# Kernel tuning notes

Measured on AMD Instinct MI355X. Metric: run time of the kernel, lower is better.

The kernel has to match this reference:

```python
import jax, jax.numpy as jnp
import numpy as np

N_LAYERS = 2
H = 16                      # num_heads
ARW = (1.0, 1.0)            # att_residual_weight
MCB = (0.0, 1.0)            # mask_clip_balancer
LN_EPS = 1e-5


def _ln(x, g, b):
    mu = jnp.mean(x, axis=-1, keepdims=True)
    var = jnp.mean(jnp.square(x - mu), axis=-1, keepdims=True)
    return (x - mu) * jax.lax.rsqrt(var + LN_EPS) * g + b


def _quick_gelu(u):
    return u * jax.nn.sigmoid(1.702 * u)


def setup_inputs() -> dict:
    key = jax.random.key(0)
    ks = jax.random.split(key, 8)
    L, B, C = 577, 8, 1024
    d_ff = 4 * C
    inp = {
        'x': jax.random.normal(ks[0], (L, B, C), jnp.float32),
        'att_bias': jax.random.normal(ks[1], (N_LAYERS, B * H, L, L), jnp.float32),
        'ln1_g': jnp.ones((N_LAYERS, C), jnp.float32),
        'ln1_b': jnp.zeros((N_LAYERS, C), jnp.float32),
        'in_w': 0.02 * jax.random.normal(ks[2], (N_LAYERS, 3 * C, C), jnp.float32),
        'in_b': jnp.zeros((N_LAYERS, 3 * C), jnp.float32),
        'out_w': 0.02 * jax.random.normal(ks[3], (N_LAYERS, C, C), jnp.float32),
        'out_b': jnp.zeros((N_LAYERS, C), jnp.float32),
        'ln2_g': jnp.ones((N_LAYERS, C), jnp.float32),
        'ln2_b': jnp.zeros((N_LAYERS, C), jnp.float32),
        'fc1_w': 0.02 * jax.random.normal(ks[4], (N_LAYERS, d_ff, C), jnp.float32),
        'fc1_b': jnp.zeros((N_LAYERS, d_ff), jnp.float32),
        'fc2_w': 0.02 * jax.random.normal(ks[5], (N_LAYERS, C, d_ff), jnp.float32),
        'fc2_b': jnp.zeros((N_LAYERS, C), jnp.float32),
    }
    return inp


def reference(x, att_bias, ln1_g, ln1_b, in_w, in_b, out_w, out_b,
              ln2_g, ln2_b, fc1_w, fc1_b, fc2_w, fc2_b):
    L, B, C = x.shape
    d = C // H
    scale = d ** -0.5  # custom_att_factor is None
    for i in range(N_LAYERS):
        # --- custom CSA attention ---
        h = _ln(x, ln1_g[i], ln1_b[i])                              # [L,B,C]
        qkv = jnp.einsum('lbc,fc->lbf', h, in_w[i]) + in_b[i]       # [L,B,3C]
        q, k, v = jnp.split(qkv, 3, axis=-1)
        to_heads = lambda t: t.reshape(L, B, H, d).transpose(1, 2, 0, 3)  # [B,H,L,d]
        q, k, v = to_heads(q), to_heads(k), to_heads(v)
        bias = att_bias[i].reshape(B, H, L, L)
        q_attn = bias + scale * jnp.einsum('bhld,bhmd->bhlm', q, q)
        k_attn = bias + scale * jnp.einsum('bhld,bhmd->bhlm', k, k)
        attn = jax.nn.softmax(q_attn, axis=-1) + jax.nn.softmax(k_attn, axis=-1)
        attn = attn * 0.5                                           # norm_att=True
        attn = jnp.mean(attn, axis=1, keepdims=True)                # avg_att=True -> [B,1,L,L]
        out = jnp.matmul(attn, v)                                   # broadcast over H -> [B,H,L,d]
        out = MCB[0] * v + MCB[1] * out
        out = out.transpose(2, 0, 1, 3).reshape(L, B, C)
        out = jnp.einsum('lbc,oc->lbo', out, out_w[i]) + out_b[i]
        x = ARW[0] * x + ARW[1] * out
        # --- MLP residual ---
        h2 = _ln(x, ln2_g[i], ln2_b[i])
        u = _quick_gelu(jnp.einsum('lbc,fc->lbf', h2, fc1_w[i]) + fc1_b[i])
        x = x + jnp.einsum('lbf,cf->lbc', u, fc2_w[i]) + fc2_b[i]
    return x
```

## Files before the change

### kernel.cpp

```cpp
#include <hip/hip_runtime.h>

typedef float f32x4 __attribute__((ext_vector_type(4)));
typedef __bf16 bf16x8 __attribute__((ext_vector_type(8)));

#define L_SEQ 577
#define BB 8
#define CC 1024
#define HH 16
#define ROWS (L_SEQ*BB)

static __device__ __forceinline__ ushort f2b(float f) {
  unsigned u = __float_as_uint(f);
  u += 0x7fffu + ((u >> 16) & 1u);
  return (ushort)(u >> 16);
}

static __device__ __forceinline__ void gld16(const void* g, void* l) {
  __builtin_amdgcn_global_load_lds((const __attribute__((address_space(1))) void*)g,
                                   (__attribute__((address_space(3))) void*)l, 16, 0, 0);
}

__global__ void cvt4_kernel(const float* __restrict__ s0, ushort* __restrict__ d0, int n0,
                            const float* __restrict__ s1, ushort* __restrict__ d1, int n1,
                            const float* __restrict__ s2, ushort* __restrict__ d2, int n2,
                            const float* __restrict__ s3, ushort* __restrict__ d3, int n3)
{
  int i = blockIdx.x * blockDim.x + threadIdx.x;
  const float* src; ushort* dst;
  if (i < n0)                { src = s0; dst = d0; }
  else if ((i -= n0) < n1)   { src = s1; dst = d1; }
  else if ((i -= n1) < n2)   { src = s2; dst = d2; }
  else if ((i -= n2) < n3)   { src = s3; dst = d3; }
  else return;
  float4 v = *(const float4*)(src + (size_t)i * 4);
  ushort4 o;
  o.x = f2b(v.x); o.y = f2b(v.y); o.z = f2b(v.z); o.w = f2b(v.w);
  *(ushort4*)(dst + (size_t)i * 4) = o;
}

template<int NP, bool DOLN>
__global__ __launch_bounds__(256)
void ln_resid_kernel(const float* __restrict__ xsrc, const float* __restrict__ parts,
                     const float* __restrict__ cbias,
                     const float* __restrict__ g, const float* __restrict__ be,
                     float* __restrict__ xdst, ushort* __restrict__ hout)
{
  const int row = blockIdx.x;
  const int t = threadIdx.x;
  float4 v = *(const float4*)(xsrc + (size_t)row * CC + t * 4);
  if (NP > 0) {
    float4 c4 = *(const float4*)(cbias + t * 4);
    v.x += c4.x; v.y += c4.y; v.z += c4.z; v.w += c4.w;
    #pragma unroll
    for (int p = 0; p < NP; ++p) {
      float4 pv = *(const float4*)(parts + ((size_t)p * ROWS + row) * CC + t * 4);
      v.x += pv.x; v.y += pv.y; v.z += pv.z; v.w += pv.w;
    }
  }
  *(float4*)(xdst + (size_t)row * CC + t * 4) = v;
  if (DOLN) {
    float s  = v.x + v.y + v.z + v.w;
    float s2 = v.x*v.x + v.y*v.y + v.z*v.z + v.w*v.w;
    #pragma unroll
    for (int sd = 1; sd < 64; sd <<= 1) { s += __shfl_xor(s, sd, 64); s2 += __shfl_xor(s2, sd, 64); }
    __shared__ float ps[4], ps2[4];
    const int w = t >> 6;
    if ((t & 63) == 0) { ps[w] = s; ps2[w] = s2; }
    __syncthreads();
    s  = ps[0] + ps[1] + ps[2] + ps[3];
    s2 = ps2[0] + ps2[1] + ps2[2] + ps2[3];
    const float mean = s * (1.f / 1024.f);
    const float var  = s2 * (1.f / 1024.f) - mean * mean;
    const float rstd = rsqrtf(var + 1e-5f);
    float4 gv = *(const float4*)(g + t * 4);
    float4 bv = *(const float4*)(be + t * 4);
    ushort4 o;
    o.x = f2b((v.x - mean) * rstd * gv.x + bv.x);
    o.y = f2b((v.y - mean) * rstd * gv.y + bv.y);
    o.z = f2b((v.z - mean) * rstd * gv.z + bv.z);
    o.w = f2b((v.w - mean) * rstd * gv.w + bv.w);
    *(ushort4*)(hout + (size_t)row * CC + t * 4) = o;
  }
}

__global__ __launch_bounds__(256)
void vt_kernel(const ushort* __restrict__ qkv, ushort* __restrict__ vt)
{
  __shared__ ushort tile[32][33];
  const int lt = blockIdx.x * 32;
  const int nt = blockIdx.y * 32;
  const int b  = blockIdx.z;
  const int tx = threadIdx.x & 31;
  const int ty = threadIdx.x >> 5;
  #pragma unroll
  for (int p = 0; p < 4; ++p) {
    int l = lt + ty + p * 8;
    ushort v = 0;
    if (l < L_SEQ) v = qkv[((size_t)l * BB + b) * 3072 + 2048 + nt + tx];
    tile[ty + p * 8][tx] = v;
  }
  __syncthreads();
  #pragma unroll
  for (int p = 0; p < 4; ++p) {
    int n = nt + ty + p * 8;
    int l = lt + tx;
    vt[((size_t)b * 1024 + n) * 608 + l] = tile[tx][ty + p * 8];
  }
}

__global__ __launch_bounds__(512, 2)
void attn_kernel(const ushort* __restrict__ qkv,
                 const float* __restrict__ bias,
                 ushort* __restrict__ attnp)
{
  __shared__ float2 red[2][2][8][16];
  __shared__ ushort sm[16][612];
  const int t = threadIdx.x;
  const int lane = t & 63;
  const int w = t >> 6;
  const int fr = lane & 15;
  const int lq = lane >> 4;
  const int id = blockIdx.x;
  const int b  = id & 7;
  const int rem = id >> 3;
  const int rb = rem % 37;
  const int hg = rem / 37;
  const int r0 = rb * 16;
  const int rowl = min(r0 + fr, L_SEQ - 1);
  const size_t rbase = ((size_t)rowl * BB + b) * 3072;
  const int kc = lq * 8;

  size_t cbs_[5];
  int c0_[5];
  #pragma unroll
  for (int it = 0; it < 5; ++it) {
    const int nt = w + it * 8;
    const int crow = min(nt * 16 + fr, L_SEQ - 1);
    cbs_[it] = ((size_t)crow * BB + b) * 3072;
    c0_[it] = nt * 16 + lq * 4;
  }

  float acc[5][4];
  #pragma unroll
  for (int it = 0; it < 5; ++it)
    #pragma unroll
    for (int r = 0; r < 4; ++r) acc[it][r] = 0.f;

  for (int h4 = 0; h4 < 4; ++h4) {
    const int h = hg * 4 + h4;
    const int qoff = h * 64;
    const int koff = CC + h * 64;
    const bf16x8 rfq0 = *(const bf16x8*)(qkv + rbase + qoff + kc);
    const bf16x8 rfq1 = *(const bf16x8*)(qkv + rbase + qoff + 32 + kc);
    const bf16x8 rfk0 = *(const bf16x8*)(qkv + rbase + koff + kc);
    const bf16x8 rfk1 = *(const bf16x8*)(qkv + rbase + koff + 32 + kc);
    const float* brow = bias + (((size_t)(b * HH + h)) * L_SEQ + rowl) * L_SEQ;

    float bs[5][4];
    #pragma unroll
    for (int it = 0; it < 5; ++it)
      #pragma unroll
      for (int r = 0; r < 4; ++r) bs[it][r] = brow[min(c0_[it] + r, L_SEQ - 1)];
    bf16x8 cq0[5], cq1[5], ck0[5], ck1[5];
    #pragma unroll
    for (int it = 0; it < 5; ++it) {
      const ushort* cp = qkv + cbs_[it];
      cq0[it] = *(const bf16x8*)(cp + qoff + kc);
      cq1[it] = *(const bf16x8*)(cp + qoff + 32 + kc);
      ck0[it] = *(const bf16x8*)(cp + koff + kc);
      ck1[it] = *(const bf16x8*)(cp + koff + 32 + kc);
    }

    float sq[5][4], sk[5][4];
    #pragma unroll
    for (int it = 0; it < 5; ++it) {
      f32x4 dq = {0.f, 0.f, 0.f, 0.f};
      f32x4 dk = {0.f, 0.f, 0.f, 0.f};
      dq = __builtin_amdgcn_mfma_f32_16x16x32_bf16(cq0[it], rfq0, dq, 0, 0, 0);
      dq = __builtin_amdgcn_mfma_f32_16x16x32_bf16(cq1[it], rfq1, dq, 0, 0, 0);
      dk = __builtin_amdgcn_mfma_f32_16x16x32_bf16(ck0[it], rfk0, dk, 0, 0, 0);
      dk = __builtin_amdgcn_mfma_f32_16x16x32_bf16(ck1[it], rfk1, dk, 0, 0, 0);
      #pragma unroll
      for (int r = 0; r < 4; ++r) {
        const bool cv = (c0_[it] + r < L_SEQ);
        sq[it][r] = cv ? (bs[it][r] + 0.125f * dq[r]) : -1e30f;
        sk[it][r] = cv ? (bs[it][r] + 0.125f * dk[r]) : -1e30f;
      }
    }
    float mwq = -1e30f, mwk = -1e30f;
    #pragma unroll
    for (int it = 0; it < 5; ++it)
      #pragma unroll
      for (int r = 0; r < 4; ++r) { mwq = fmaxf(mwq, sq[it][r]); mwk = fmaxf(mwk, sk[it][r]); }
    mwq = fmaxf(mwq, __shfl_xor(mwq, 16, 64)); mwq = fmaxf(mwq, __shfl_xor(mwq, 32, 64));
    mwk = fmaxf(mwk, __shfl_xor(mwk, 16, 64)); mwk = fmaxf(mwk, __shfl_xor(mwk, 32, 64));
    float swq = 0.f, swk = 0.f;
    #pragma unroll
    for (int it = 0; it < 5; ++it)
      #pragma unroll
      for (int r = 0; r < 4; ++r) {
        sq[it][r] = __expf(sq[it][r] - mwq); swq += sq[it][r];
        sk[it][r] = __expf(sk[it][r] - mwk); swk += sk[it][r];
      }
    swq += __shfl_xor(swq, 16, 64); swq += __shfl_xor(swq, 32, 64);
    swk += __shfl_xor(swk, 16, 64); swk += __shfl_xor(swk, 32, 64);
    const int p = h4 & 1;
    if (lane < 16) {
      red[p][0][w][lane] = make_float2(mwq, swq);
      red[p][1][w][lane] = make_float2(mwk, swk);
    }
    __syncthreads();
    float mq = -1e30f, mk = -1e30f;
    #pragma unroll
    for (int ww = 0; ww < 8; ++ww) {
      mq = fmaxf(mq, red[p][0][ww][fr].x);
      mk = fmaxf(mk, red[p][1][ww][fr].x);
    }
    float smq = 0.f, smk = 0.f;
    #pragma unroll
    for (int ww = 0; ww < 8; ++ww) {
      const float2 pq = red[p][0][ww][fr];
      const float2 pk = red[p][1][ww][fr];
      smq += pq.y * __expf(pq.x - mq);
      smk += pk.y * __expf(pk.x - mk);
    }
    const float fq = 0.03125f * __expf(mwq - mq) / smq;
    const float fk = 0.03125f * __expf(mwk - mk) / smk;
    #pragma unroll
    for (int it = 0; it < 5; ++it)
      #pragma unroll
      for (int r = 0; r < 4; ++r) acc[it][r] += sq[it][r] * fq + sk[it][r] * fk;
  }

  #pragma unroll
  for (int it = 0; it < 5; ++it) {
    if (c0_[it] < 608) {
      ushort4 o;
      o.x = f2b(acc[it][0]); o.y = f2b(acc[it][1]);
      o.z = f2b(acc[it][2]); o.w = f2b(acc[it][3]);
      *(ushort4*)&sm[fr][c0_[it]] = o;
    }
  }
  __syncthreads();
  ushort* dst = attnp + ((size_t)hg * 8 + b) * 608 * 608 + (size_t)r0 * 608;
  for (int j = t; j < 16 * 152; j += 512) {
    const int row = j / 152;
    const int c4 = (j % 152) * 4;
    if (r0 + row < L_SEQ)
      *(ushort4*)(dst + (size_t)row * 608 + c4) = *(const ushort4*)&sm[row][c4];
  }
}

__global__ __launch_bounds__(256)
void attn_combine(const ushort* __restrict__ attnp, ushort* __restrict__ attn)
{
  const int t = threadIdx.x;
  if (t >= 152) return;
  const int l = blockIdx.x;
  const int b = blockIdx.y;
  const int c0 = t * 4;
  const size_t base = ((size_t)b * 608 + l) * 608 + c0;
  const size_t hs = (size_t)8 * 608 * 608;
  float s[4] = {0.f, 0.f, 0.f, 0.f};
  #pragma unroll
  for (int p = 0; p < 4; ++p) {
    ushort4 v = *(const ushort4*)(attnp + p * hs + base);
    s[0] += __uint_as_float((unsigned)v.x << 16);
    s[1] += __uint_as_float((unsigned)v.y << 16);
    s[2] += __uint_as_float((unsigned)v.z << 16);
    s[3] += __uint_as_float((unsigned)v.w << 16);
  }
  ushort4 o;
  const bool lv = (l < L_SEQ);
  o.x = (lv && c0 + 0 < L_SEQ) ? f2b(s[0]) : (ushort)0;
  o.y = (lv && c0 + 1 < L_SEQ) ? f2b(s[1]) : (ushort)0;
  o.z = (lv && c0 + 2 < L_SEQ) ? f2b(s[2]) : (ushort)0;
  o.w = (lv && c0 + 3 < L_SEQ) ? f2b(s[3]) : (ushort)0;
  *(ushort4*)(attn + base) = o;
}

__global__ __launch_bounds__(256, 2)
void av_gemm(const ushort* __restrict__ A, int lda, int Arows, long aStride,
             const ushort* __restrict__ B, int ldb, long bStride,
             int M, int K,
             ushort* __restrict__ outb, int ldo)
{
  __shared__ __align__(16) ushort As[128 * 32];
  __shared__ __align__(16) ushort Bs[128 * 32];
  const int t = threadIdx.x;
  const int lane = t & 63;
  const int w = t >> 6;
  const int bm = blockIdx.x, bn = blockIdx.y, bz = blockIdx.z;
  const ushort* Ab = A + (long)bz * aStride;
  const ushort* Bb = B + (long)bz * bStride;
  const int srow = t >> 2;
  const int sc = (t & 3) * 8;
  const int wr = (w >> 1) * 64;
  const int wc = (w & 1) * 64;
  const int am1 = Arows - 1;
  f32x4 acc[4][4] = {};

  const int r0a = bm * 128 + srow;
  const int r0b = bn * 128 + srow;
  for (int kt = 0; kt < K; kt += 32) {
    __syncthreads();
    gld16(Ab + (size_t)min(r0a, am1) * lda + kt + sc, (void*)(As + t * 8));
    gld16(Ab + (size_t)min(r0a + 64, am1) * lda + kt + sc, (void*)(As + 2048 + t * 8));
    gld16(Bb + (size_t)r0b * ldb + kt + sc, (void*)(Bs + t * 8));
    gld16(Bb + (size_t)(r0b + 64) * ldb + kt + sc, (void*)(Bs + 2048 + t * 8));
    asm volatile("s_waitcnt vmcnt(0)" ::: "memory");
    __syncthreads();
    bf16x8 av[4], bv[4];
    const int fr = lane & 15;
    const int kc = (lane >> 4) * 8;
    #pragma unroll
    for (int m = 0; m < 4; ++m) av[m] = *(const bf16x8*)(As + (wr + m * 16 + fr) * 32 + kc);
    #pragma unroll
    for (int n = 0; n < 4; ++n) bv[n] = *(const bf16x8*)(Bs + (wc + n * 16 + fr) * 32 + kc);
    #pragma unroll
    for (int m = 0; m < 4; ++m)
      #pragma unroll
      for (int n = 0; n < 4; ++n)
        acc[m][n] = __builtin_amdgcn_mfma_f32_16x16x32_bf16(av[m], bv[n], acc[m][n], 0, 0, 0);
  }
  const int rbase = wr + (lane >> 4) * 4;
  const int cbase = wc + (lane & 15);
  #pragma unroll
  for (int n = 0; n < 4; ++n) {
    const int gn = bn * 128 + cbase + n * 16;
    #pragma unroll
    for (int m = 0; m < 4; ++m) {
      f32x4 d = acc[m][n];
      #pragma unroll
      for (int r = 0; r < 4; ++r) {
        const int gm = bm * 128 + rbase + m * 16 + r;
        if (gm < M) outb[((size_t)gm * 8 + bz) * ldo + gn] = f2b(d[r]);
      }
    }
  }
}

#define RD_A8(BOFS, MH) \
  _Pragma("unroll") for (int ks = 0; ks < 2; ++ks) \
  _Pragma("unroll") for (int m = 0; m < 4; ++m) \
    Af[ks][m] = rdA(BOFS, MH, ks, m);

#define RD_B4(BOFS, NH) \
  _Pragma("unroll") for (int ks = 0; ks < 2; ++ks) \
  _Pragma("unroll") for (int n = 0; n < 2; ++n) \
    Bf[NH][ks][n] = rdB(BOFS, NH, ks, n);

#define MFQ(MH, NH) \
  _Pragma("unroll") for (int ks = 0; ks < 2; ++ks) \
  _Pragma("unroll") for (int m = 0; m < 4; ++m) \
  _Pragma("unroll") for (int n = 0; n < 2; ++n) \
    acc[(MH)*4+m][(NH)*2+n] = __builtin_amdgcn_mfma_f32_16x16x32_bf16( \
        Af[ks][m], Bf[NH][ks][n], acc[(MH)*4+m][(NH)*2+n], 0, 0, 0);

#define BARO() \
  __builtin_amdgcn_sched_barrier(0); \
  __builtin_amdgcn_s_barrier(); \
  asm volatile("s_waitcnt lgkmcnt(0)" ::: "memory"); \
  __builtin_amdgcn_sched_barrier(0); \
  __builtin_amdgcn_s_setprio(1);

#define MF_END() \
  __builtin_amdgcn_s_setprio(0); \
  __builtin_amdgcn_sched_barrier(0); \
  __builtin_amdgcn_s_barrier();

template<int EPI>
__global__ __launch_bounds__(512, 2)
void gemm8(const ushort* __restrict__ Ap, int lda, int Arows,
           const ushort* __restrict__ Bp, int ldb,
           int M, int Ksplit,
           const float* __restrict__ bias,
           ushort* __restrict__ outb, float* __restrict__ outf, int ldo)
{
  __shared__ __align__(16) char smem[131072];
  const int t = threadIdx.x;
  const int lane = t & 63;
  const int w = t >> 6;
  const int wm = w >> 2, wn = w & 3;
  const int gx = gridDim.x;
  const int nwg = gx * gridDim.y;
  int id = blockIdx.y * gx + blockIdx.x;
  {
    const int q8 = nwg >> 3, r8 = nwg & 7;
    const int xcd = id & 7, pos = id >> 3;
    id = (xcd < r8 ? xcd * (q8 + 1) : r8 * (q8 + 1) + (xcd - r8) * q8) + pos;
  }
  const int bm = id % gx, bn = id / gx;
  const int bz = blockIdx.z;
  const int k0 = bz * Ksplit;
  const int iters = Ksplit >> 7;
  const int fr = lane & 15, lq = lane >> 4;

  f32x4 acc[8][4] = {};
  bf16x8 Af[2][4];
  bf16x8 Bf[2][2][2];

  const int rowj0 = t >> 3,        cbj0 = t & 7;
  const int rowj1 = (t + 512) >> 3, cbj1 = (t + 512) & 7;
  const ushort* pA[2][2]; const ushort* pB[2][2];
  #pragma unroll
  for (int h = 0; h < 2; ++h) {
    pA[h][0] = Ap + (size_t)min(bm*256 + h*128 + rowj0, Arows-1) * lda + k0 + ((cbj0 ^ (rowj0 & 7)) << 3);
    pA[h][1] = Ap + (size_t)min(bm*256 + h*128 + rowj1, Arows-1) * lda + k0 + ((cbj1 ^ (rowj1 & 7)) << 3);
    pB[h][0] = Bp + (size_t)(bn*256 + h*128 + rowj0) * ldb + k0 + ((cbj0 ^ (rowj0 & 7)) << 3);
    pB[h][1] = Bp + (size_t)(bn*256 + h*128 + rowj1) * ldb + k0 + ((cbj1 ^ (rowj1 & 7)) << 3);
  }

  auto stA = [&](int kt, int bofs, int h) {
    gld16(pA[h][0] + kt * 64, smem + bofs + h * 16384 + t * 16);
    gld16(pA[h][1] + kt * 64, smem + bofs + h * 16384 + (t + 512) * 16);
  };
  auto stB = [&](int kt, int bofs, int h) {
    gld16(pB[h][0] + kt * 64, smem + bofs + 32768 + h * 16384 + t * 16);
    gld16(pB[h][1] + kt * 64, smem + bofs + 32768 + h * 16384 + (t + 512) * 16);
  };
  auto rdA = [&](int bofs, int mh, int ks, int m) -> bf16x8 {
    const int rl = wm * 64 + m * 16 + fr;
    const int cb = (ks * 4 + lq) ^ (fr & 7);
    return *(const bf16x8*)(smem + bofs + mh * 16384 + rl * 128 + cb * 16);
  };
  auto rdB = [&](int bofs, int nh, int ks, int n) -> bf16x8 {
    const int rl = wn * 32 + n * 16 + fr;
    const int cb = (ks * 4 + lq) ^ (fr & 7);
    return *(const bf16x8*)(smem + bofs + 32768 + nh * 16384 + rl * 128 + cb * 16);
  };

  stA(0, 0, 0); stB(0, 0, 0); stB(0, 0, 1); stA(0, 0, 1);
  stA(1, 65536, 0); stB(1, 65536, 1); stA(1, 65536, 1);
  asm volatile("s_waitcnt vmcnt(6)" ::: "memory");
  __builtin_amdgcn_sched_barrier(0);
  __builtin_amdgcn_s_barrier();

  for (int i = 0; i < iters; ++i) {
    const bool more = (i + 1 < iters);
    const int kt2 = 2 * i + 2;
    RD_A8(0, 0) RD_B4(0, 0)
    stB(2 * i + 1, 65536, 0);
    BARO(); MFQ(0, 0) MF_END();
    RD_B4(0, 1)
    if (more) stA(kt2, 0, 0);
    BARO(); MFQ(0, 1) MF_END();
    RD_A8(0, 1)
    if (more) stB(kt2, 0, 1);
    BARO(); MFQ(1, 1) MF_END();
    if (more) stA(kt2, 0, 1);
    BARO(); MFQ(1, 0)
    __builtin_amdgcn_s_setprio(0);
    if (more) { asm volatile("s_waitcnt vmcnt(6)" ::: "memory"); }
    else      { asm volatile("s_waitcnt vmcnt(0)" ::: "memory"); }
    __builtin_amdgcn_sched_barrier(0);
    __builtin_amdgcn_s_barrier();
    RD_A8(65536, 0) RD_B4(65536, 0)
    if (more) stB(kt2, 0, 0);
    BARO(); MFQ(0, 0) MF_END();
    RD_B4(65536, 1)
    if (more) stA(2 * i + 3, 65536, 0);
    BARO(); MFQ(0, 1) MF_END();
    RD_A8(65536, 1)
    if (more) stB(2 * i + 3, 65536, 1);
    BARO(); MFQ(1, 1) MF_END();
    if (more) stA(2 * i + 3, 65536, 1);
    BARO(); MFQ(1, 0)
    __builtin_amdgcn_s_setprio(0);
    if (more) { asm volatile("s_waitcnt vmcnt(6)" ::: "memory"); }
    __builtin_amdgcn_sched_barrier(0);
    __builtin_amdgcn_s_barrier();
  }

  #pragma unroll
  for (int mh = 0; mh < 2; ++mh)
  #pragma unroll
  for (int nh = 0; nh < 2; ++nh)
  #pragma unroll
  for (int n = 0; n < 2; ++n) {
    const int gn = bn * 256 + nh * 128 + wn * 32 + n * 16 + fr;
    const float bval = (EPI == 4) ? 0.f : bias[gn];
    #pragma unroll
    for (int m = 0; m < 4; ++m) {
      f32x4 d = acc[mh * 4 + m][nh * 2 + n];
      #pragma unroll
      for (int r = 0; r < 4; ++r) {
        const int gm = bm * 256 + mh * 128 + wm * 64 + m * 16 + lq * 4 + r;
        if (gm < M) {
          if (EPI == 0) {
            outb[(size_t)gm * ldo + gn] = f2b(d[r] + bval);
          } else if (EPI == 1) {
            float v0 = d[r] + bval;
            outb[(size_t)gm * ldo + gn] = f2b(v0 / (1.f + __expf(-1.702f * v0)));
          } else {
            outf[((size_t)bz * M + gm) * ldo + gn] = d[r];
          }
        }
      }
    }
  }
}

extern "C" void kernel_launch(void* const* d_in, const int* in_sizes, int n_in,
                              void* d_out, int out_size, void* d_ws, size_t ws_size,
                              hipStream_t stream)
{
  (void)in_sizes; (void)n_in; (void)out_size; (void)ws_size;
  const float* x_in  = (const float*)d_in[0];
  const float* attb  = (const float*)d_in[1];
  const float* ln1_g = (const float*)d_in[2];
  const float* ln1_b = (const float*)d_in[3];
  const float* in_w  = (const float*)d_in[4];
  const float* in_b  = (const float*)d_in[5];
  const float* out_w = (const float*)d_in[6];
  const float* out_b = (const float*)d_in[7];
  const float* ln2_g = (const float*)d_in[8];
  const float* ln2_b = (const float*)d_in[9];
  const float* fc1_w = (const float*)d_in[10];
  const float* fc1_b = (const float*)d_in[11];
  const float* fc2_w = (const float*)d_in[12];
  const float* fc2_b = (const float*)d_in[13];
  float* x = (float*)d_out;

  char* ws = (char*)d_ws;
  size_t off = 0;
  auto alloc = [&](size_t bytes) -> void* {
    void* p = ws + off; off += (bytes + 255) & ~(size_t)255; return p;
  };
  ushort* wIn   = (ushort*)alloc(2ull * 3072 * 1024 * 2);
  ushort* wOut  = (ushort*)alloc(2ull * 1024 * 1024 * 2);
  ushort* wF1   = (ushort*)alloc(2ull * 4096 * 1024 * 2);
  ushort* wF2   = (ushort*)alloc(2ull * 4096 * 1024 * 2);
  ushort* hbuf  = (ushort*)alloc((size_t)ROWS * 1024 * 2);
  ushort* qkv   = (ushort*)alloc((size_t)ROWS * 3072 * 2);
  ushort* vt    = (ushort*)alloc((size_t)8 * 1024 * 608 * 2);
  ushort* attn  = (ushort*)alloc((size_t)8 * 608 * 608 * 2);
  ushort* attnp = (ushort*)alloc((size_t)4 * 8 * 608 * 608 * 2);
  ushort* outlb = (ushort*)alloc((size_t)ROWS * 1024 * 2);
  float*  pbuf  = (float*)alloc((size_t)4 * ROWS * 1024 * 4);
  ushort* ubuf  = qkv;

  cvt4_kernel<<<(1572864 + 524288 + 2097152 + 2097152 + 255) / 256, 256, 0, stream>>>(
      in_w,  wIn,  1572864,
      out_w, wOut, 524288,
      fc1_w, wF1,  2097152,
      fc2_w, wF2,  2097152);
  ln_resid_kernel<0, true><<<ROWS, 256, 0, stream>>>(x_in, nullptr, nullptr,
      ln1_g, ln1_b, x, hbuf);

  for (int i = 0; i < 2; ++i) {
    gemm8<0><<<dim3(19, 12, 1), 512, 0, stream>>>(hbuf, 1024, ROWS,
        wIn + (size_t)i * 3072 * 1024, 1024,
        ROWS, 1024, in_b + i * 3072, qkv, nullptr, 3072);
    attn_kernel<<<dim3(1184, 1, 1), 512, 0, stream>>>(qkv, attb + (size_t)i * 128 * 577 * 577, attnp);
    vt_kernel<<<dim3(19, 32, 8), 256, 0, stream>>>(qkv, vt);
    attn_combine<<<dim3(608, 8), 256, 0, stream>>>(attnp, attn);
    av_gemm<<<dim3(5, 8, 8), 256, 0, stream>>>(attn, 608, 577, (long)608 * 608,
        vt, 608, (long)1024 * 608, 577, 608, outlb, 1024);
    gemm8<4><<<dim3(19, 4, 2), 512, 0, stream>>>(outlb, 1024, ROWS,
        wOut + (size_t)i * 1024 * 1024, 1024,
        ROWS, 512, nullptr, nullptr, pbuf, 1024);
    ln_resid_kernel<2, true><<<ROWS, 256, 0, stream>>>(x, pbuf, out_b + i * 1024,
        ln2_g + i * 1024, ln2_b + i * 1024, x, hbuf);
    gemm8<1><<<dim3(19, 16, 1), 512, 0, stream>>>(hbuf, 1024, ROWS,
        wF1 + (size_t)i * 4096 * 1024, 1024,
        ROWS, 1024, fc1_b + i * 4096, ubuf, nullptr, 4096);
    gemm8<4><<<dim3(19, 4, 4), 512, 0, stream>>>(ubuf, 4096, ROWS,
        wF2 + (size_t)i * 4096 * 1024, 4096,
        ROWS, 1024, nullptr, nullptr, pbuf, 1024);
    if (i == 0) {
      ln_resid_kernel<4, true><<<ROWS, 256, 0, stream>>>(x, pbuf, fc2_b,
          ln1_g + 1024, ln1_b + 1024, x, hbuf);
    } else {
      ln_resid_kernel<4, false><<<ROWS, 256, 0, stream>>>(x, pbuf, fc2_b + 1024,
          nullptr, nullptr, x, nullptr);
    }
  }
}
```

Measured before the change: 1.022 ms.

## Process 32 query rows per attention block, reusing column fragments across row tiles

The attention-score kernel now handles two 16-row tiles per block (32 rows), so each loaded column fragment of Q/K feeds two MFMAs and the grid halves from 1184 to 608 blocks. Q and K softmaxes are processed sequentially with a software-pipelined, double-buffered prefetch of column fragments instead of loading all five at once. This reduces redundant global loads of column data per row and lowers register pressure for fragments, but doubles accumulator and bias registers and adds an extra block barrier per head, and the smaller grid may reduce occupancy and latency hiding.

```diff
diff --git a/kernel.cpp b/kernel.cpp
--- a/kernel.cpp
+++ b/kernel.cpp
@@ -114,7 +114,7 @@
                  ushort* __restrict__ attnp)
 {
   __shared__ float2 red[2][2][8][16];
-  __shared__ ushort sm[16][612];
+  __shared__ ushort sm[32][612];
   const int t = threadIdx.x;
   const int lane = t & 63;
   const int w = t >> 6;
@@ -123,15 +123,18 @@
   const int id = blockIdx.x;
   const int b  = id & 7;
   const int rem = id >> 3;
-  const int rb = rem % 37;
-  const int hg = rem / 37;
-  const int r0 = rb * 16;
-  const int rowl = min(r0 + fr, L_SEQ - 1);
-  const size_t rbase = ((size_t)rowl * BB + b) * 3072;
+  const int rb = rem % 19;
+  const int hg = rem / 19;
+  const int r0 = rb * 32;
   const int kc = lq * 8;
 
-  size_t cbs_[5];
-  int c0_[5];
+  int rowl[2]; size_t rbase[2];
+  #pragma unroll
+  for (int rs = 0; rs < 2; ++rs) {
+    rowl[rs] = min(r0 + rs * 16 + fr, L_SEQ - 1);
+    rbase[rs] = ((size_t)rowl[rs] * BB + b) * 3072;
+  }
+  size_t cbs_[5]; int c0_[5];
   #pragma unroll
   for (int it = 0; it < 5; ++it) {
     const int nt = w + it * 8;
@@ -140,110 +143,121 @@
     c0_[it] = nt * 16 + lq * 4;
   }
 
-  float acc[5][4];
-  #pragma unroll
-  for (int it = 0; it < 5; ++it)
-    #pragma unroll
-    for (int r = 0; r < 4; ++r) acc[it][r] = 0.f;
+  float acc[2][5][4];
+  #pragma unroll
+  for (int rs = 0; rs < 2; ++rs)
+    #pragma unroll
+    for (int it = 0; it < 5; ++it)
+      #pragma unroll
+      for (int r = 0; r < 4; ++r) acc[rs][it][r] = 0.f;
 
   for (int h4 = 0; h4 < 4; ++h4) {
     const int h = hg * 4 + h4;
-    const int qoff = h * 64;
-    const int koff = CC + h * 64;
-    const bf16x8 rfq0 = *(const bf16x8*)(qkv + rbase + qoff + kc);
-    const bf16x8 rfq1 = *(const bf16x8*)(qkv + rbase + qoff + 32 + kc);
-    const bf16x8 rfk0 = *(const bf16x8*)(qkv + rbase + koff + kc);
-    const bf16x8 rfk1 = *(const bf16x8*)(qkv + rbase + koff + 32 + kc);
-    const float* brow = bias + (((size_t)(b * HH + h)) * L_SEQ + rowl) * L_SEQ;
-
-    float bs[5][4];
+    const float* brow0 = bias + (((size_t)(b * HH + h)) * L_SEQ + rowl[0]) * L_SEQ;
+    const float* brow1 = bias + (((size_t)(b * HH + h)) * L_SEQ + rowl[1]) * L_SEQ;
+    float bs[2][5][4];
     #pragma unroll
     for (int it = 0; it < 5; ++it)
       #pragma unroll
-      for (int r = 0; r < 4; ++r) bs[it][r] = brow[min(c0_[it] + r, L_SEQ - 1)];
-    bf16x8 cq0[5], cq1[5], ck0[5], ck1[5];
+      for (int r = 0; r < 4; ++r) {
+        const int cc = min(c0_[it] + r, L_SEQ - 1);
+        bs[0][it][r] = brow0[cc];
+        bs[1][it][r] = brow1[cc];
+      }
+    #pragma unroll
+    for (int v = 0; v < 2; ++v) {
+      const int off = (v ? CC : 0) + h * 64;
+      bf16x8 rf0[2], rf1[2];
+      #pragma unroll
+      for (int rs = 0; rs < 2; ++rs) {
+        rf0[rs] = *(const bf16x8*)(qkv + rbase[rs] + off + kc);
+        rf1[rs] = *(const bf16x8*)(qkv + rbase[rs] + off + 32 + kc);
+      }
+      bf16x8 cA0 = *(const bf16x8*)(qkv + cbs_[0] + off + kc);
+      bf16x8 cA1 = *(const bf16x8*)(qkv + cbs_[0] + off + 32 + kc);
+      bf16x8 cB0 = *(const bf16x8*)(qkv + cbs_[1] + off + kc);
+      bf16x8 cB1 = *(const bf16x8*)(qkv + cbs_[1] + off + 32 + kc);
+      float s[2][5][4];
+      #pragma unroll
+      for (int it = 0; it < 5; ++it) {
+        const bf16x8 c0f = cA0, c1f = cA1;
+        cA0 = cB0; cA1 = cB1;
+        if (it + 2 < 5) {
+          cB0 = *(const bf16x8*)(qkv + cbs_[it + 2] + off + kc);
+          cB1 = *(const bf16x8*)(qkv + cbs_[it + 2] + off + 32 + kc);
+        }
+        f32x4 d0 = {0.f, 0.f, 0.f, 0.f};
+        f32x4 d1 = {0.f, 0.f, 0.f, 0.f};
+        d0 = __builtin_amdgcn_mfma_f32_16x16x32_bf16(c0f, rf0[0], d0, 0, 0, 0);
+        d0 = __builtin_amdgcn_mfma_f32_16x16x32_bf16(c1f, rf1[0], d0, 0, 0, 0);
+        d1 = __builtin_amdgcn_mfma_f32_16x16x32_bf16(c0f, rf0[1], d1, 0, 0, 0);
+        d1 = __builtin_amdgcn_mfma_f32_16x16x32_bf16(c1f, rf1[1], d1, 0, 0, 0);
+        #pragma unroll
+        for (int r = 0; r < 4; ++r) {
+          const bool cv = (c0_[it] + r < L_SEQ);
+          s[0][it][r] = cv ? (bs[0][it][r] + 0.125f * d0[r]) : -1e30f;
+          s[1][it][r] = cv ? (bs[1][it][r] + 0.125f * d1[r]) : -1e30f;
+        }
+      }
+      float mw[2], sw[2];
+      #pragma unroll
+      for (int rs = 0; rs < 2; ++rs) {
+        float m = -1e30f;
+        #pragma unroll
+        for (int it = 0; it < 5; ++it)
+          #pragma unroll
+          for (int r = 0; r < 4; ++r) m = fmaxf(m, s[rs][it][r]);
+        m = fmaxf(m, __shfl_xor(m, 16, 64));
+        m = fmaxf(m, __shfl_xor(m, 32, 64));
+        float sum = 0.f;
+        #pragma unroll
+        for (int it = 0; it < 5; ++it)
+          #pragma unroll
+          for (int r = 0; r < 4; ++r) { s[rs][it][r] = __expf(s[rs][it][r] - m); sum += s[rs][it][r]; }
+        sum += __shfl_xor(sum, 16, 64);
+        sum += __shfl_xor(sum, 32, 64);
+        mw[rs] = m; sw[rs] = sum;
+      }
+      const int p = (h4 * 2 + v) & 1;
+      if (lane < 16) {
+        red[p][0][w][lane] = make_float2(mw[0], sw[0]);
+        red[p][1][w][lane] = make_float2(mw[1], sw[1]);
+      }
+      __syncthreads();
+      #pragma unroll
+      for (int rs = 0; rs < 2; ++rs) {
+        float m = -1e30f;
+        #pragma unroll
+        for (int ww = 0; ww < 8; ++ww) m = fmaxf(m, red[p][rs][ww][fr].x);
+        float smm = 0.f;
+        #pragma unroll
+        for (int ww = 0; ww < 8; ++ww) {
+          const float2 q = red[p][rs][ww][fr];
+          smm += q.y * __expf(q.x - m);
+        }
+        const float f = 0.03125f * __expf(mw[rs] - m) / smm;
+        #pragma unroll
+        for (int it = 0; it < 5; ++it)
+          #pragma unroll
+          for (int r = 0; r < 4; ++r) acc[rs][it][r] += s[rs][it][r] * f;
+      }
+    }
+  }
+
+  #pragma unroll
+  for (int rs = 0; rs < 2; ++rs)
     #pragma unroll
     for (int it = 0; it < 5; ++it) {
-      const ushort* cp = qkv + cbs_[it];
-      cq0[it] = *(const bf16x8*)(cp + qoff + kc);
-      cq1[it] = *(const bf16x8*)(cp + qoff + 32 + kc);
-      ck0[it] = *(const bf16x8*)(cp + koff + kc);
-      ck1[it] = *(const bf16x8*)(cp + koff + 32 + kc);
+      if (c0_[it] < 608) {
+        ushort4 o;
+        o.x = f2b(acc[rs][it][0]); o.y = f2b(acc[rs][it][1]);
+        o.z = f2b(acc[rs][it][2]); o.w = f2b(acc[rs][it][3]);
+        *(ushort4*)&sm[rs * 16 + fr][c0_[it]] = o;
+      }
     }
-
-    float sq[5][4], sk[5][4];
-    #pragma unroll
-    for (int it = 0; it < 5; ++it) {
-      f32x4 dq = {0.f, 0.f, 0.f, 0.f};
-      f32x4 dk = {0.f, 0.f, 0.f, 0.f};
-      dq = __builtin_amdgcn_mfma_f32_16x16x32_bf16(cq0[it], rfq0, dq, 0, 0, 0);
-      dq = __builtin_amdgcn_mfma_f32_16x16x32_bf16(cq1[it], rfq1, dq, 0, 0, 0);
-      dk = __builtin_amdgcn_mfma_f32_16x16x32_bf16(ck0[it], rfk0, dk, 0, 0, 0);
-      dk = __builtin_amdgcn_mfma_f32_16x16x32_bf16(ck1[it], rfk1, dk, 0, 0, 0);
-      #pragma unroll
-      for (int r = 0; r < 4; ++r) {
-        const bool cv = (c0_[it] + r < L_SEQ);
-        sq[it][r] = cv ? (bs[it][r] + 0.125f * dq[r]) : -1e30f;
-        sk[it][r] = cv ? (bs[it][r] + 0.125f * dk[r]) : -1e30f;
-      }
-    }
-    float mwq = -1e30f, mwk = -1e30f;
-    #pragma unroll
-    for (int it = 0; it < 5; ++it)
-      #pragma unroll
-      for (int r = 0; r < 4; ++r) { mwq = fmaxf(mwq, sq[it][r]); mwk = fmaxf(mwk, sk[it][r]); }
-    mwq = fmaxf(mwq, __shfl_xor(mwq, 16, 64)); mwq = fmaxf(mwq, __shfl_xor(mwq, 32, 64));
-    mwk = fmaxf(mwk, __shfl_xor(mwk, 16, 64)); mwk = fmaxf(mwk, __shfl_xor(mwk, 32, 64));
-    float swq = 0.f, swk = 0.f;
-    #pragma unroll
-    for (int it = 0; it < 5; ++it)
-      #pragma unroll
-      for (int r = 0; r < 4; ++r) {
-        sq[it][r] = __expf(sq[it][r] - mwq); swq += sq[it][r];
-        sk[it][r] = __expf(sk[it][r] - mwk); swk += sk[it][r];
-      }
-    swq += __shfl_xor(swq, 16, 64); swq += __shfl_xor(swq, 32, 64);
-    swk += __shfl_xor(swk, 16, 64); swk += __shfl_xor(swk, 32, 64);
-    const int p = h4 & 1;
-    if (lane < 16) {
-      red[p][0][w][lane] = make_float2(mwq, swq);
-      red[p][1][w][lane] = make_float2(mwk, swk);
-    }
-    __syncthreads();
-    float mq = -1e30f, mk = -1e30f;
-    #pragma unroll
-    for (int ww = 0; ww < 8; ++ww) {
-      mq = fmaxf(mq, red[p][0][ww][fr].x);
-      mk = fmaxf(mk, red[p][1][ww][fr].x);
-    }
-    float smq = 0.f, smk = 0.f;
-    #pragma unroll
-    for (int ww = 0; ww < 8; ++ww) {
-      const float2 pq = red[p][0][ww][fr];
-      const float2 pk = red[p][1][ww][fr];
-      smq += pq.y * __expf(pq.x - mq);
-      smk += pk.y * __expf(pk.x - mk);
-    }
-    const float fq = 0.03125f * __expf(mwq - mq) / smq;
-    const float fk = 0.03125f * __expf(mwk - mk) / smk;
-    #pragma unroll
-    for (int it = 0; it < 5; ++it)
-      #pragma unroll
-      for (int r = 0; r < 4; ++r) acc[it][r] += sq[it][r] * fq + sk[it][r] * fk;
-  }
-
-  #pragma unroll
-  for (int it = 0; it < 5; ++it) {
-    if (c0_[it] < 608) {
-      ushort4 o;
-      o.x = f2b(acc[it][0]); o.y = f2b(acc[it][1]);
-      o.z = f2b(acc[it][2]); o.w = f2b(acc[it][3]);
-      *(ushort4*)&sm[fr][c0_[it]] = o;
-    }
-  }
   __syncthreads();
   ushort* dst = attnp + ((size_t)hg * 8 + b) * 608 * 608 + (size_t)r0 * 608;
-  for (int j = t; j < 16 * 152; j += 512) {
+  for (int j = t; j < 32 * 152; j += 512) {
     const int row = j / 152;
     const int c4 = (j % 152) * 4;
     if (r0 + row < L_SEQ)
@@ -552,7 +566,7 @@
     gemm8<0><<<dim3(19, 12, 1), 512, 0, stream>>>(hbuf, 1024, ROWS,
         wIn + (size_t)i * 3072 * 1024, 1024,
         ROWS, 1024, in_b + i * 3072, qkv, nullptr, 3072);
-    attn_kernel<<<dim3(1184, 1, 1), 512, 0, stream>>>(qkv, attb + (size_t)i * 128 * 577 * 577, attnp);
+    attn_kernel<<<dim3(608, 1, 1), 512, 0, stream>>>(qkv, attb + (size_t)i * 128 * 577 * 577, attnp);
     vt_kernel<<<dim3(19, 32, 8), 256, 0, stream>>>(qkv, vt);
     attn_combine<<<dim3(608, 8), 256, 0, stream>>>(attnp, attn);
     av_gemm<<<dim3(5, 8, 8), 256, 0, stream>>>(attn, 608, 577, (long)608 * 608,
```

After: 998.3 us. 1.02x faster.
